# Kernel optimization log

Measured on AMD Instinct MI355X. Metric: run time of the kernel, lower is better.

The kernel has to match this reference:

```python
import jax, jax.numpy as jnp
import numpy as np

N = 8192
N_DIM = 7
N_WIDTH = 64


def setup_inputs() -> dict:
    key = jax.random.key(0)
    ks = jax.random.split(key, 12)
    scale = 0.05
    u = lambda k, shape: scale * (2.0 * jax.random.uniform(k, shape) - 1.0)
    # Linear params stored as (in, out) so forward uses x @ W + b (same math as torch Linear).
    lin = lambda k, fan_in, fan_out: (
        jax.random.uniform(jax.random.fold_in(k, 0), (fan_in, fan_out),
                           minval=-1.0, maxval=1.0) / np.sqrt(fan_in),
        jax.random.uniform(jax.random.fold_in(k, 1), (fan_out,),
                           minval=-1.0, maxval=1.0) / np.sqrt(fan_in),
    )
    W1, b1 = lin(ks[1], N_DIM, N_WIDTH)
    W2, b2 = lin(ks[2], N_WIDTH, N_WIDTH)
    Wl, bl = lin(ks[3], N_WIDTH, 1)
    return {
        "x": jax.random.normal(ks[0], (N, N_DIM), dtype=jnp.float32),
        "alpha": jax.random.uniform(ks[4], (1,)),          # Edges.alpha = 1 * rand(1)
        "W1": W1, "b1": b1, "wt1": u(ks[5], (N_WIDTH, N_WIDTH)), "bs1": u(ks[6], (1,)),
        "W2": W2, "b2": b2, "wt2": u(ks[7], (N_WIDTH, N_WIDTH)), "bs2": u(ks[8], (1,)),
        "Wl": Wl, "bl": bl,
    }


def _edges(x, alpha):
    eta, phi = x[:, 1], x[:, 2]
    deta = eta[:, None] - eta[None, :]                      # (n, n)
    dphi = jnp.abs(phi[:, None] - phi[None, :])
    dphi = jnp.where(dphi > jnp.pi, 2.0 * jnp.pi - dphi, dphi)
    dRdR = deta * deta + dphi * dphi
    A = jnp.exp(-alpha[0] * dRdR)
    return jax.nn.softmax(A, axis=1) + jnp.eye(x.shape[0], dtype=x.dtype)


def _gcn_layer(X, A, W, b, wt, bs):
    X = jax.nn.relu(X @ W + b)                              # embed + relu
    X = (A @ X) @ wt + bs[0]                                # aggregate + mix + scalar bias
    return jax.nn.relu(X)


def reference(x, alpha, W1, b1, wt1, bs1, W2, b2, wt2, bs2, Wl, bl):
    A = _edges(x, alpha)
    V = jax.nn.relu(_gcn_layer(x, A, W1, b1, wt1, bs1))
    V = jax.nn.relu(_gcn_layer(V, A, W2, b2, wt2, bs2))
    s = V.sum(axis=0)                                       # (n_width,)
    return jax.nn.sigmoid(s @ Wl + bl)                      # (1,)
```

## Files before the change

kernel.cpp:

```cpp
#include <hip/hip_runtime.h>
#include <math.h>

#define NN 8192
#define L2E 1.44269504088896340736f
#define TWO_PI 6.28318530717958647693f

typedef _Float16 h8 __attribute__((ext_vector_type(8)));
typedef _Float16 h4 __attribute__((ext_vector_type(4)));
typedef float f32x4 __attribute__((ext_vector_type(4)));
typedef float f32x2 __attribute__((ext_vector_type(2)));
#define MFMA16(A, B, C) __builtin_amdgcn_mfma_f32_16x16x32_f16(A, B, C, 0, 0, 0)

#define GLD_LDS16(gsrc, ldst)                                          \
  __builtin_amdgcn_global_load_lds(                                    \
      (const __attribute__((address_space(1))) unsigned int*)(gsrc),   \
      (__attribute__((address_space(3))) unsigned int*)(ldst), 16, 0, 0)

union V8 { float4 v[2]; float f[8]; };

__global__ __launch_bounds__(256) void prep_kernel(
    const float* __restrict__ x, const float* __restrict__ alpha,
    const float* __restrict__ W1, const float* __restrict__ b1,
    float* __restrict__ eta_s, float* __restrict__ phi_s,
    float* __restrict__ H1, _Float16* __restrict__ HT1,
    float* __restrict__ svec)
{
  __shared__ float sW[448];
  __shared__ float sb[64];
  __shared__ float T[32][68];
  const int t = threadIdx.x;
  if (blockIdx.x == 0 && t < 64) svec[t] = 0.f;
  for (int k = t; k < 448; k += 256) sW[k] = W1[k];
  if (t < 64) sb[t] = b1[t];
  const float s = sqrtf(alpha[0] * L2E);
  const int i0 = blockIdx.x * 32;
  const int r = t >> 3, q = t & 7;
  const int i = i0 + r;
  float xv[7];
#pragma unroll
  for (int k = 0; k < 7; k++) xv[k] = x[i * 7 + k];
  if (q == 0) { eta_s[i] = xv[1] * s; phi_s[i] = xv[2] * s; }
  __syncthreads();
#pragma unroll
  for (int c = 0; c < 8; c++) {
    const int n = q * 8 + c;
    float hv = sb[n];
#pragma unroll
    for (int k = 0; k < 7; k++) hv = fmaf(xv[k], sW[k * 64 + n], hv);
    T[r][n] = fmaxf(hv, 0.f);
  }
  __syncthreads();
  for (int e = t; e < 512; e += 256)
    *(f32x4*)(H1 + (size_t)i0 * 64 + (e << 2)) =
        *(const f32x4*)&T[e >> 4][(e << 2) & 63];
  const int n = t >> 2, sg = (t & 3) * 8;
  h8 v;
#pragma unroll
  for (int ss = 0; ss < 8; ss++) v[ss] = (_Float16)T[sg + ss][n];
  *(h8*)(HT1 + (size_t)n * NN + i0 + sg) = v;
}

template <bool NEED_L>
__global__ __launch_bounds__(256, 4) void attn_pass(
    const float* __restrict__ eta_s, const float* __restrict__ phi_s,
    const _Float16* __restrict__ HT, const float* __restrict__ alpha,
    float* __restrict__ Ypart, float* __restrict__ lpart)
{
  __shared__ __align__(16) char smem[32768];
  _Float16* stage = (_Float16*)smem;
  const int tid = threadIdx.x;
  const int w = tid >> 6, lane = tid & 63, m = lane & 15, g = lane >> 4;
  const int tile = blockIdx.x >> 2, part = blockIdx.x & 3;
  const int i0 = tile << 5;
  const int jbase = part << 11;
  const float Cs = TWO_PI * sqrtf(alpha[0] * L2E);
  const float et0 = eta_s[i0 + m],      ph0 = phi_s[i0 + m];
  const float et1 = eta_s[i0 + 16 + m], ph1 = phi_s[i0 + 16 + m];

  const int r0 = tid >> 4, gq = tid & 15;
  const _Float16* sbase = HT + (size_t)r0 * NN + ((gq ^ r0) << 3) + jbase;

  f32x4 a00 = {0,0,0,0}, a01 = {0,0,0,0}, a02 = {0,0,0,0}, a03 = {0,0,0,0};
  f32x4 a10 = {0,0,0,0}, a11 = {0,0,0,0}, a12 = {0,0,0,0}, a13 = {0,0,0,0};
  f32x4 l0a = {0,0,0,0}, l1a = {0,0,0,0};
  const h8 onesv = {(_Float16)1.f, (_Float16)1.f, (_Float16)1.f, (_Float16)1.f,
                    (_Float16)1.f, (_Float16)1.f, (_Float16)1.f, (_Float16)1.f};

  const float* ep = eta_s + jbase + (w << 5) + (g << 3);
  const float* pp = phi_s + jbase + (w << 5) + (g << 3);
  V8 E0, P0, E1, P1;
  E0.v[0] = *(const float4*)ep;  E0.v[1] = *(const float4*)(ep + 4);
  P0.v[0] = *(const float4*)pp;  P0.v[1] = *(const float4*)(pp + 4);

#pragma unroll
  for (int k = 0; k < 4; ++k)
    GLD_LDS16(sbase + (size_t)k * 16 * NN, stage + ((k * 256 + tid) << 3));
  __syncthreads();

  const int fs = ((m << 4) + (((w << 2) | g) ^ m)) << 3;

  union AF { h8 v; decltype(__builtin_amdgcn_cvt_pkrtz(0.f, 0.f)) p[4]; };

  auto stage_compute = [&](const V8& Ec, const V8& Pc, const _Float16* cur) {
    const h8 b0 = *(const h8*)(cur + fs);
    const h8 b1 = *(const h8*)(cur + 2048 + fs);
    const h8 b2 = *(const h8*)(cur + 4096 + fs);
    const h8 b3 = *(const h8*)(cur + 6144 + fs);
    AF af0, af1;
#pragma unroll
    for (int tt = 0; tt < 8; tt += 2) {
      const f32x2 pj = {Pc.f[tt], Pc.f[tt + 1]};
      const f32x2 ej = {Ec.f[tt], Ec.f[tt + 1]};
      const f32x2 dp0 = ph0 - pj, dp1 = ph1 - pj;
      const f32x2 ad0 = {fabsf(dp0.x), fabsf(dp0.y)};
      const f32x2 ad1 = {fabsf(dp1.x), fabsf(dp1.y)};
      const f32x2 cm0 = Cs - ad0, cm1 = Cs - ad1;
      const f32x2 wr0 = {fminf(ad0.x, cm0.x), fminf(ad0.y, cm0.y)};
      const f32x2 wr1 = {fminf(ad1.x, cm1.x), fminf(ad1.y, cm1.y)};
      const f32x2 de0 = et0 - ej, de1 = et1 - ej;
      const f32x2 r20 = de0 * de0 + wr0 * wr0;
      const f32x2 r21 = de1 * de1 + wr1 * wr1;
      const f32x2 ax0 = {__builtin_amdgcn_exp2f(-r20.x),
                         __builtin_amdgcn_exp2f(-r20.y)};
      const f32x2 ax1 = {__builtin_amdgcn_exp2f(-r21.x),
                         __builtin_amdgcn_exp2f(-r21.y)};
      const f32x2 ga0 = ax0 * L2E - L2E;
      const f32x2 ga1 = ax1 * L2E - L2E;
      af0.p[tt >> 1] = __builtin_amdgcn_cvt_pkrtz(
          __builtin_amdgcn_exp2f(ga0.x), __builtin_amdgcn_exp2f(ga0.y));
      af1.p[tt >> 1] = __builtin_amdgcn_cvt_pkrtz(
          __builtin_amdgcn_exp2f(ga1.x), __builtin_amdgcn_exp2f(ga1.y));
    }
    __builtin_amdgcn_s_setprio(1);
    a00 = MFMA16(af0.v, b0, a00); a01 = MFMA16(af0.v, b1, a01);
    a02 = MFMA16(af0.v, b2, a02); a03 = MFMA16(af0.v, b3, a03);
    a10 = MFMA16(af1.v, b0, a10); a11 = MFMA16(af1.v, b1, a11);
    a12 = MFMA16(af1.v, b2, a12); a13 = MFMA16(af1.v, b3, a13);
    if constexpr (NEED_L) {
      l0a = MFMA16(af0.v, onesv, l0a);
      l1a = MFMA16(af1.v, onesv, l1a);
    }
    __builtin_amdgcn_s_setprio(0);
  };

#pragma unroll
  for (int s2 = 0; s2 < 8; ++s2) {
    {
      const _Float16* src = sbase + (2 * s2 + 1) * 128;
#pragma unroll
      for (int k = 0; k < 4; ++k)
        GLD_LDS16(src + (size_t)k * 16 * NN,
                  stage + 8192 + ((k * 256 + tid) << 3));
      E1.v[0] = *(const float4*)(ep + s2 * 256 + 128);
      E1.v[1] = *(const float4*)(ep + s2 * 256 + 132);
      P1.v[0] = *(const float4*)(pp + s2 * 256 + 128);
      P1.v[1] = *(const float4*)(pp + s2 * 256 + 132);
      stage_compute(E0, P0, stage);
      __syncthreads();
    }
    {
      if (s2 < 7) {
        const _Float16* src = sbase + (2 * s2 + 2) * 128;
#pragma unroll
        for (int k = 0; k < 4; ++k)
          GLD_LDS16(src + (size_t)k * 16 * NN,
                    stage + ((k * 256 + tid) << 3));
        E0.v[0] = *(const float4*)(ep + s2 * 256 + 256);
        E0.v[1] = *(const float4*)(ep + s2 * 256 + 260);
        P0.v[0] = *(const float4*)(pp + s2 * 256 + 256);
        P0.v[1] = *(const float4*)(pp + s2 * 256 + 260);
      }
      stage_compute(E1, P1, stage + 8192);
      __syncthreads();
    }
  }

  typedef float Red2[32][66];
  Red2* red = (Red2*)smem;
  const int h = w >> 1;
  if ((w & 1) == 0) {
#pragma unroll
    for (int r = 0; r < 4; ++r) {
      red[h][g * 4 + r][m]      = a00[r]; red[h][g * 4 + r][16 + m] = a01[r];
      red[h][g * 4 + r][32 + m] = a02[r]; red[h][g * 4 + r][48 + m] = a03[r];
      red[h][16 + g * 4 + r][m]      = a10[r]; red[h][16 + g * 4 + r][16 + m] = a11[r];
      red[h][16 + g * 4 + r][32 + m] = a12[r]; red[h][16 + g * 4 + r][48 + m] = a13[r];
    }
    if constexpr (NEED_L) {
      if (m == 0) {
#pragma unroll
        for (int r = 0; r < 4; ++r) {
          red[h][g * 4 + r][64]      = l0a[r];
          red[h][16 + g * 4 + r][64] = l1a[r];
        }
      }
    }
  }
  __syncthreads();
  if (w & 1) {
#pragma unroll
    for (int r = 0; r < 4; ++r) {
      red[h][g * 4 + r][m]      += a00[r]; red[h][g * 4 + r][16 + m] += a01[r];
      red[h][g * 4 + r][32 + m] += a02[r]; red[h][g * 4 + r][48 + m] += a03[r];
      red[h][16 + g * 4 + r][m]      += a10[r]; red[h][16 + g * 4 + r][16 + m] += a11[r];
      red[h][16 + g * 4 + r][32 + m] += a12[r]; red[h][16 + g * 4 + r][48 + m] += a13[r];
    }
    if constexpr (NEED_L) {
      if (m == 0) {
#pragma unroll
        for (int r = 0; r < 4; ++r) {
          red[h][g * 4 + r][64]      += l0a[r];
          red[h][16 + g * 4 + r][64] += l1a[r];
        }
      }
    }
  }
  __syncthreads();
#pragma unroll
  for (int k = 0; k < 8; ++k) {
    const int e = tid + k * 256;
    Ypart[((size_t)part * NN + i0 + (e >> 6)) * 64 + (e & 63)] =
        red[0][e >> 6][e & 63] + red[1][e >> 6][e & 63];
  }
  if constexpr (NEED_L) {
    if (tid < 32)
      lpart[(size_t)part * NN + i0 + tid] = red[0][tid][64] + red[1][tid][64];
  }
}

__global__ __launch_bounds__(256) void mid_kernel(
    const float* __restrict__ Yp, const float* __restrict__ lp,
    const float* __restrict__ H1, const float* __restrict__ wt1,
    const float* __restrict__ bs1, const float* __restrict__ W2,
    const float* __restrict__ b2, float* __restrict__ H2,
    _Float16* __restrict__ HT2)
{
  __shared__ float sA[64][68];
  __shared__ float sB[64][68];
  __shared__ float U[16][68];
  __shared__ float sb2v[64];
  const int t = threadIdx.x;
  for (int e = t; e < 1024; e += 256) {
    const int rr = e >> 4, cc = (e << 2) & 63;
    *(f32x4*)&sA[rr][cc] = *(const f32x4*)(wt1 + (e << 2));
    *(f32x4*)&sB[rr][cc] = *(const f32x4*)(W2 + (e << 2));
  }
  if (t < 64) sb2v[t] = b2[t];
  const float bsv = bs1[0];
  const int i0 = blockIdx.x * 16;
  const int r = t >> 4, q = t & 15;
  const int i = i0 + r;
  float l = 0.f;
#pragma unroll
  for (int p = 0; p < 4; ++p) l += lp[(size_t)p * NN + i];
  const float rl = 1.0f / l;
  f32x4 ya = {0, 0, 0, 0};
#pragma unroll
  for (int p = 0; p < 4; ++p)
    ya += *(const f32x4*)(Yp + ((size_t)p * NN + i) * 64 + q * 4);
  const f32x4 h1 = *(const f32x4*)(H1 + (size_t)i * 64 + q * 4);
#pragma unroll
  for (int c = 0; c < 4; ++c) U[r][q * 4 + c] = fmaf(ya[c], rl, h1[c]);
  __syncthreads();
  float z[4];
#pragma unroll
  for (int c = 0; c < 4; ++c) z[c] = bsv;
#pragma unroll
  for (int k4 = 0; k4 < 64; k4 += 4) {
    const f32x4 u4 = *(const f32x4*)&U[r][k4];
#pragma unroll
    for (int kk = 0; kk < 4; ++kk) {
      const f32x4 sa = *(const f32x4*)&sA[k4 + kk][q * 4];
#pragma unroll
      for (int c = 0; c < 4; ++c) z[c] = fmaf(u4[kk], sa[c], z[c]);
    }
  }
  __syncthreads();
#pragma unroll
  for (int c = 0; c < 4; ++c) U[r][q * 4 + c] = fmaxf(z[c], 0.f);
  __syncthreads();
  float hv[4];
#pragma unroll
  for (int c = 0; c < 4; ++c) hv[c] = sb2v[q * 4 + c];
#pragma unroll
  for (int k4 = 0; k4 < 64; k4 += 4) {
    const f32x4 u4 = *(const f32x4*)&U[r][k4];
#pragma unroll
    for (int kk = 0; kk < 4; ++kk) {
      const f32x4 sb4 = *(const f32x4*)&sB[k4 + kk][q * 4];
#pragma unroll
      for (int c = 0; c < 4; ++c) hv[c] = fmaf(u4[kk], sb4[c], hv[c]);
    }
  }
  __syncthreads();
#pragma unroll
  for (int c = 0; c < 4; ++c) U[r][q * 4 + c] = fmaxf(hv[c], 0.f);
  __syncthreads();
  *(f32x4*)(H2 + (size_t)i0 * 64 + (t << 2)) =
      *(const f32x4*)&U[t >> 4][(t << 2) & 63];
  const int n = t >> 2, sg = (t & 3) * 4;
  h4 v;
#pragma unroll
  for (int ss = 0; ss < 4; ss++) v[ss] = (_Float16)U[sg + ss][n];
  *(h4*)(HT2 + (size_t)n * NN + i0 + sg) = v;
}

__global__ __launch_bounds__(256) void final_kernel(
    const float* __restrict__ Yp, const float* __restrict__ lp,
    const float* __restrict__ H2, const float* __restrict__ wt2,
    const float* __restrict__ bs2, float* __restrict__ svec)
{
  __shared__ float sA[64][68];
  __shared__ float U[16][68];
  __shared__ float cred[4][64];
  const int t = threadIdx.x;
  for (int e = t; e < 1024; e += 256) {
    const int rr = e >> 4, cc = (e << 2) & 63;
    *(f32x4*)&sA[rr][cc] = *(const f32x4*)(wt2 + (e << 2));
  }
  const float bsv = bs2[0];
  const int i0 = blockIdx.x * 16;
  const int r = t >> 4, q = t & 15;
  const int i = i0 + r;
  float l = 0.f;
#pragma unroll
  for (int p = 0; p < 4; ++p) l += lp[(size_t)p * NN + i];
  const float rl = 1.0f / l;
  f32x4 ya = {0, 0, 0, 0};
#pragma unroll
  for (int p = 0; p < 4; ++p)
    ya += *(const f32x4*)(Yp + ((size_t)p * NN + i) * 64 + q * 4);
  const f32x4 h2 = *(const f32x4*)(H2 + (size_t)i * 64 + q * 4);
#pragma unroll
  for (int c = 0; c < 4; ++c) U[r][q * 4 + c] = fmaf(ya[c], rl, h2[c]);
  __syncthreads();
  float z[4];
#pragma unroll
  for (int c = 0; c < 4; ++c) z[c] = bsv;
#pragma unroll
  for (int k4 = 0; k4 < 64; k4 += 4) {
    const f32x4 u4 = *(const f32x4*)&U[r][k4];
#pragma unroll
    for (int kk = 0; kk < 4; ++kk) {
      const f32x4 sa = *(const f32x4*)&sA[k4 + kk][q * 4];
#pragma unroll
      for (int c = 0; c < 4; ++c) z[c] = fmaf(u4[kk], sa[c], z[c]);
    }
  }
  __syncthreads();
#pragma unroll
  for (int c = 0; c < 4; ++c) U[r][q * 4 + c] = fmaxf(z[c], 0.f);
  __syncthreads();
  const int col = t & 63, rg = t >> 6;
  float ps = 0.f;
#pragma unroll
  for (int rr = 0; rr < 4; rr++) ps += U[rg * 4 + rr][col];
  cred[rg][col] = ps;
  __syncthreads();
  if (t < 64)
    atomicAdd(svec + t, cred[0][t] + cred[1][t] + cred[2][t] + cred[3][t]);
}

__global__ void out_kernel(const float* __restrict__ svec,
                           const float* __restrict__ Wl,
                           const float* __restrict__ bl,
                           float* __restrict__ out)
{
  const int t = threadIdx.x;
  float v = svec[t] * Wl[t];
#pragma unroll
  for (int off = 32; off > 0; off >>= 1) v += __shfl_down(v, off);
  if (t == 0) {
    const float logit = v + bl[0];
    out[0] = 1.0f / (1.0f + __builtin_amdgcn_exp2f(-logit * L2E));
  }
}

extern "C" void kernel_launch(void* const* d_in, const int* in_sizes, int n_in,
                              void* d_out, int out_size, void* d_ws,
                              size_t ws_size, hipStream_t stream)
{
  const float* x     = (const float*)d_in[0];
  const float* alpha = (const float*)d_in[1];
  const float* W1    = (const float*)d_in[2];
  const float* b1    = (const float*)d_in[3];
  const float* wt1   = (const float*)d_in[4];
  const float* bs1   = (const float*)d_in[5];
  const float* W2    = (const float*)d_in[6];
  const float* b2    = (const float*)d_in[7];
  const float* wt2   = (const float*)d_in[8];
  const float* bs2   = (const float*)d_in[9];
  const float* Wl    = (const float*)d_in[10];
  const float* bl    = (const float*)d_in[11];
  float* out = (float*)d_out;

  char* ws = (char*)d_ws;
  size_t off = 0;
  auto alloc = [&](size_t bytes) {
    void* p = ws + off;
    off = (off + bytes + 255) & ~(size_t)255;
    return p;
  };
  float* eta_s = (float*)alloc(NN * 4 + 256);
  float* phi_s = (float*)alloc(NN * 4 + 256);
  float* H1    = (float*)alloc((size_t)NN * 64 * 4);
  float* H2    = (float*)alloc((size_t)NN * 64 * 4);
  float* Ypart = (float*)alloc((size_t)4 * NN * 64 * 4);
  float* lpart = (float*)alloc((size_t)4 * NN * 4);
  _Float16* HT = (_Float16*)alloc((size_t)NN * 64 * 2 + 512);
  float* svec  = (float*)alloc(64 * 4);

  prep_kernel<<<256, 256, 0, stream>>>(x, alpha, W1, b1, eta_s, phi_s, H1, HT, svec);
  attn_pass<true><<<1024, 256, 0, stream>>>(eta_s, phi_s, HT, alpha, Ypart, lpart);
  mid_kernel<<<512, 256, 0, stream>>>(Ypart, lpart, H1, wt1, bs1, W2, b2, H2, HT);
  attn_pass<false><<<1024, 256, 0, stream>>>(eta_s, phi_s, HT, alpha, Ypart, nullptr);
  final_kernel<<<512, 256, 0, stream>>>(Ypart, lpart, H2, wt2, bs2, svec);
  out_kernel<<<1, 64, 0, stream>>>(svec, Wl, bl, out);
}
```

Before: 167.5 us.

## Materialize fp16 edge weights in pass one and reuse them in pass two

The first attention pass now stores the computed fp16 exponentiated edge weights into a full NxN global buffer. The second pass loads these weights instead of recomputing the distance and exp math, and only performs the MFMA aggregation. This trades transcendental/VALU work in pass two for 128MB of extra global writes and reads, plus a large workspace allocation.

New measurement: 172.6 us. 1.03x slower.

```diff
diff --git a/kernel.cpp b/kernel.cpp
--- a/kernel.cpp
+++ b/kernel.cpp
@@ -60,10 +60,11 @@
   *(h8*)(HT1 + (size_t)n * NN + i0 + sg) = v;
 }
 
-template <bool NEED_L>
+template <bool PASS1>
 __global__ __launch_bounds__(256, 4) void attn_pass(
     const float* __restrict__ eta_s, const float* __restrict__ phi_s,
     const _Float16* __restrict__ HT, const float* __restrict__ alpha,
+    _Float16* __restrict__ Pm,
     float* __restrict__ Ypart, float* __restrict__ lpart)
 {
   __shared__ __align__(16) char smem[32768];
@@ -73,9 +74,7 @@
   const int tile = blockIdx.x >> 2, part = blockIdx.x & 3;
   const int i0 = tile << 5;
   const int jbase = part << 11;
-  const float Cs = TWO_PI * sqrtf(alpha[0] * L2E);
-  const float et0 = eta_s[i0 + m],      ph0 = phi_s[i0 + m];
-  const float et1 = eta_s[i0 + 16 + m], ph1 = phi_s[i0 + 16 + m];
+  const int jcol0 = jbase + (w << 5) + (g << 3);
 
   const int r0 = tid >> 4, gq = tid & 15;
   const _Float16* sbase = HT + (size_t)r0 * NN + ((gq ^ r0) << 3) + jbase;
@@ -86,11 +85,26 @@
   const h8 onesv = {(_Float16)1.f, (_Float16)1.f, (_Float16)1.f, (_Float16)1.f,
                     (_Float16)1.f, (_Float16)1.f, (_Float16)1.f, (_Float16)1.f};
 
-  const float* ep = eta_s + jbase + (w << 5) + (g << 3);
-  const float* pp = phi_s + jbase + (w << 5) + (g << 3);
+  _Float16* const pw0 = Pm + (size_t)(i0 + m) * NN + jcol0;
+  _Float16* const pw1 = Pm + (size_t)(i0 + 16 + m) * NN + jcol0;
+
+  float Cs = 0.f, et0 = 0.f, ph0 = 0.f, et1 = 0.f, ph1 = 0.f;
+  const float* ep = nullptr;
+  const float* pp = nullptr;
   V8 E0, P0, E1, P1;
-  E0.v[0] = *(const float4*)ep;  E0.v[1] = *(const float4*)(ep + 4);
-  P0.v[0] = *(const float4*)pp;  P0.v[1] = *(const float4*)(pp + 4);
+  h8 pe0, pe1, po0, po1;
+  if constexpr (PASS1) {
+    Cs = TWO_PI * sqrtf(alpha[0] * L2E);
+    et0 = eta_s[i0 + m];      ph0 = phi_s[i0 + m];
+    et1 = eta_s[i0 + 16 + m]; ph1 = phi_s[i0 + 16 + m];
+    ep = eta_s + jcol0;
+    pp = phi_s + jcol0;
+    E0.v[0] = *(const float4*)ep;  E0.v[1] = *(const float4*)(ep + 4);
+    P0.v[0] = *(const float4*)pp;  P0.v[1] = *(const float4*)(pp + 4);
+  } else {
+    pe0 = *(const h8*)(pw0);        pe1 = *(const h8*)(pw1);
+    po0 = *(const h8*)(pw0 + 128);  po1 = *(const h8*)(pw1 + 128);
+  }
 
 #pragma unroll
   for (int k = 0; k < 4; ++k)
@@ -101,7 +115,8 @@
 
   union AF { h8 v; decltype(__builtin_amdgcn_cvt_pkrtz(0.f, 0.f)) p[4]; };
 
-  auto stage_compute = [&](const V8& Ec, const V8& Pc, const _Float16* cur) {
+  auto stage_compute = [&](const V8& Ec, const V8& Pc, const _Float16* cur,
+                           int sIdx) {
     const h8 b0 = *(const h8*)(cur + fs);
     const h8 b1 = *(const h8*)(cur + 2048 + fs);
     const h8 b2 = *(const h8*)(cur + 4096 + fs);
@@ -131,15 +146,28 @@
       af1.p[tt >> 1] = __builtin_amdgcn_cvt_pkrtz(
           __builtin_amdgcn_exp2f(ga1.x), __builtin_amdgcn_exp2f(ga1.y));
     }
+    *(h8*)(pw0 + sIdx * 128) = af0.v;
+    *(h8*)(pw1 + sIdx * 128) = af1.v;
     __builtin_amdgcn_s_setprio(1);
     a00 = MFMA16(af0.v, b0, a00); a01 = MFMA16(af0.v, b1, a01);
     a02 = MFMA16(af0.v, b2, a02); a03 = MFMA16(af0.v, b3, a03);
     a10 = MFMA16(af1.v, b0, a10); a11 = MFMA16(af1.v, b1, a11);
     a12 = MFMA16(af1.v, b2, a12); a13 = MFMA16(af1.v, b3, a13);
-    if constexpr (NEED_L) {
-      l0a = MFMA16(af0.v, onesv, l0a);
-      l1a = MFMA16(af1.v, onesv, l1a);
-    }
+    l0a = MFMA16(af0.v, onesv, l0a);
+    l1a = MFMA16(af1.v, onesv, l1a);
+    __builtin_amdgcn_s_setprio(0);
+  };
+
+  auto stage_gemm = [&](h8 af0v, h8 af1v, const _Float16* cur) {
+    const h8 b0 = *(const h8*)(cur + fs);
+    const h8 b1 = *(const h8*)(cur + 2048 + fs);
+    const h8 b2 = *(const h8*)(cur + 4096 + fs);
+    const h8 b3 = *(const h8*)(cur + 6144 + fs);
+    __builtin_amdgcn_s_setprio(1);
+    a00 = MFMA16(af0v, b0, a00); a01 = MFMA16(af0v, b1, a01);
+    a02 = MFMA16(af0v, b2, a02); a03 = MFMA16(af0v, b3, a03);
+    a10 = MFMA16(af1v, b0, a10); a11 = MFMA16(af1v, b1, a11);
+    a12 = MFMA16(af1v, b2, a12); a13 = MFMA16(af1v, b3, a13);
     __builtin_amdgcn_s_setprio(0);
   };
 
@@ -151,11 +179,20 @@
       for (int k = 0; k < 4; ++k)
         GLD_LDS16(src + (size_t)k * 16 * NN,
                   stage + 8192 + ((k * 256 + tid) << 3));
-      E1.v[0] = *(const float4*)(ep + s2 * 256 + 128);
-      E1.v[1] = *(const float4*)(ep + s2 * 256 + 132);
-      P1.v[0] = *(const float4*)(pp + s2 * 256 + 128);
-      P1.v[1] = *(const float4*)(pp + s2 * 256 + 132);
-      stage_compute(E0, P0, stage);
+      if constexpr (PASS1) {
+        E1.v[0] = *(const float4*)(ep + s2 * 256 + 128);
+        E1.v[1] = *(const float4*)(ep + s2 * 256 + 132);
+        P1.v[0] = *(const float4*)(pp + s2 * 256 + 128);
+        P1.v[1] = *(const float4*)(pp + s2 * 256 + 132);
+        stage_compute(E0, P0, stage, 2 * s2);
+      } else {
+        const h8 c0 = pe0, c1 = pe1;
+        if (s2 < 7) {
+          pe0 = *(const h8*)(pw0 + (2 * s2 + 2) * 128);
+          pe1 = *(const h8*)(pw1 + (2 * s2 + 2) * 128);
+        }
+        stage_gemm(c0, c1, stage);
+      }
       __syncthreads();
     }
     {
@@ -165,12 +202,23 @@
         for (int k = 0; k < 4; ++k)
           GLD_LDS16(src + (size_t)k * 16 * NN,
                     stage + ((k * 256 + tid) << 3));
-        E0.v[0] = *(const float4*)(ep + s2 * 256 + 256);
-        E0.v[1] = *(const float4*)(ep + s2 * 256 + 260);
-        P0.v[0] = *(const float4*)(pp + s2 * 256 + 256);
-        P0.v[1] = *(const float4*)(pp + s2 * 256 + 260);
+        if constexpr (PASS1) {
+          E0.v[0] = *(const float4*)(ep + s2 * 256 + 256);
+          E0.v[1] = *(const float4*)(ep + s2 * 256 + 260);
+          P0.v[0] = *(const float4*)(pp + s2 * 256 + 256);
+          P0.v[1] = *(const float4*)(pp + s2 * 256 + 260);
+        }
       }
-      stage_compute(E1, P1, stage + 8192);
+      if constexpr (PASS1) {
+        stage_compute(E1, P1, stage + 8192, 2 * s2 + 1);
+      } else {
+        const h8 c0 = po0, c1 = po1;
+        if (s2 < 7) {
+          po0 = *(const h8*)(pw0 + (2 * s2 + 3) * 128);
+          po1 = *(const h8*)(pw1 + (2 * s2 + 3) * 128);
+        }
+        stage_gemm(c0, c1, stage + 8192);
+      }
       __syncthreads();
     }
   }
@@ -186,7 +234,7 @@
       red[h][16 + g * 4 + r][m]      = a10[r]; red[h][16 + g * 4 + r][16 + m] = a11[r];
       red[h][16 + g * 4 + r][32 + m] = a12[r]; red[h][16 + g * 4 + r][48 + m] = a13[r];
     }
-    if constexpr (NEED_L) {
+    if constexpr (PASS1) {
       if (m == 0) {
 #pragma unroll
         for (int r = 0; r < 4; ++r) {
@@ -205,7 +253,7 @@
       red[h][16 + g * 4 + r][m]      += a10[r]; red[h][16 + g * 4 + r][16 + m] += a11[r];
       red[h][16 + g * 4 + r][32 + m] += a12[r]; red[h][16 + g * 4 + r][48 + m] += a13[r];
     }
-    if constexpr (NEED_L) {
+    if constexpr (PASS1) {
       if (m == 0) {
 #pragma unroll
         for (int r = 0; r < 4; ++r) {
@@ -222,7 +270,7 @@
     Ypart[((size_t)part * NN + i0 + (e >> 6)) * 64 + (e & 63)] =
         red[0][e >> 6][e & 63] + red[1][e >> 6][e & 63];
   }
-  if constexpr (NEED_L) {
+  if constexpr (PASS1) {
     if (tid < 32)
       lpart[(size_t)part * NN + i0 + tid] = red[0][tid][64] + red[1][tid][64];
   }
@@ -409,11 +457,12 @@
   float* lpart = (float*)alloc((size_t)4 * NN * 4);
   _Float16* HT = (_Float16*)alloc((size_t)NN * 64 * 2 + 512);
   float* svec  = (float*)alloc(64 * 4);
+  _Float16* Pm = (_Float16*)alloc((size_t)NN * NN * 2);
 
   prep_kernel<<<256, 256, 0, stream>>>(x, alpha, W1, b1, eta_s, phi_s, H1, HT, svec);
-  attn_pass<true><<<1024, 256, 0, stream>>>(eta_s, phi_s, HT, alpha, Ypart, lpart);
+  attn_pass<true><<<1024, 256, 0, stream>>>(eta_s, phi_s, HT, alpha, Pm, Ypart, lpart);
   mid_kernel<<<512, 256, 0, stream>>>(Ypart, lpart, H1, wt1, bs1, W2, b2, H2, HT);
-  attn_pass<false><<<1024, 256, 0, stream>>>(eta_s, phi_s, HT, alpha, Ypart, nullptr);
+  attn_pass<false><<<1024, 256, 0, stream>>>(eta_s, phi_s, HT, alpha, Pm, Ypart, nullptr);
   final_kernel<<<512, 256, 0, stream>>>(Ypart, lpart, H2, wt2, bs2, svec);
   out_kernel<<<1, 64, 0, stream>>>(svec, Wl, bl, out);
 }
```
